# Optimization experiments

Hardware: AMD Instinct MI355X
Metric: run time of the kernel (lower is better)

Reference implementation:

```python
import jax, jax.numpy as jnp
import numpy as np

HID = 256        # constant.hidden_size
EMB = 256        # constant.embedding_size
STATE_NUM = 5    # constant.state_num
PAD_ID = 0


def _lstm(x, Wih, Whh, b):
    # x: (N, T, D) -> (N, T, H); single-layer unidirectional, PyTorch gate order i,f,g,o
    N = x.shape[0]
    Hh = Whh.shape[1]
    def step(carry, xt):
        h, c = carry
        g = xt @ Wih.T + h @ Whh.T + b
        i, f, gg, o = jnp.split(g, 4, axis=-1)
        c = jax.nn.sigmoid(f) * c + jax.nn.sigmoid(i) * jnp.tanh(gg)
        h = jax.nn.sigmoid(o) * jnp.tanh(c)
        return (h, c), h
    h0 = jnp.zeros((N, Hh), x.dtype)
    _, ys = jax.lax.scan(step, (h0, h0), jnp.swapaxes(x, 0, 1))
    return jnp.swapaxes(ys, 0, 1)


def setup_inputs() -> dict:
    rng = np.random.RandomState(0)
    B, L, W, V = 8, 128, 48, 50000
    S = STATE_NUM
    P = L // (S - 1)
    batch_utterances = jnp.asarray(rng.randint(0, V, size=(B, L, W)), jnp.int32)
    utterance_sequence_length = jnp.asarray(rng.randint(1, W + 1, size=(B, L)), jnp.int32)
    perm = np.stack([b * L + rng.permutation(L) for b in range(B)]).reshape(-1)
    session_transpose_matrix = jnp.asarray(perm, jnp.int32)
    stm = np.zeros((B, L, S), np.int32)  # col 0 == 0 -> new-state slot (projection path)
    carry = rng.rand(B, L, S - 1) < 0.3
    pos = rng.randint(1, P + 1, size=(B, L, S - 1))
    stm[:, :, 1:] = np.where(carry, -1, pos)
    state_transition_matrix = jnp.asarray(stm)

    def w(*shape):
        return jnp.asarray(rng.randn(*shape) * 0.05, jnp.float32)

    return dict(
        batch_utterances=batch_utterances,
        utterance_sequence_length=utterance_sequence_length,
        session_transpose_matrix=session_transpose_matrix,
        state_transition_matrix=state_transition_matrix,
        max_conversation_length=L,
        emb=w(V, EMB),
        utt_Wih=w(4 * HID, EMB), utt_Whh=w(4 * HID, HID), utt_b=w(4 * HID),
        ws1=w(HID, HID), ws2=w(1, HID),
        conv_Wih=w(4 * HID, HID), conv_Whh=w(4 * HID, HID), conv_b=w(4 * HID),
        sess_Wih=w(4 * HID, HID), sess_Whh=w(4 * HID, HID), sess_b=w(4 * HID),
        Wp=w(HID, 2 * HID), bp=w(HID),
        Ws=w(HID, 2 * HID), bs=w(HID),
    )


def reference(batch_utterances, utterance_sequence_length, session_transpose_matrix,
              state_transition_matrix, max_conversation_length,
              emb, utt_Wih, utt_Whh, utt_b, ws1, ws2,
              conv_Wih, conv_Whh, conv_b, sess_Wih, sess_Whh, sess_b,
              Wp, bp, Ws, bs):
    B, L, W = batch_utterances.shape
    S = STATE_NUM
    P = L // (S - 1)
    Lc = int(max_conversation_length)

    # --- UtteranceEncoder: embedding lookup + word-level LSTM ---
    tok = batch_utterances.reshape(-1, W)            # (B*L, W)
    word_out = _lstm(emb[tok], utt_Wih, utt_Whh, utt_b)  # (B*L, W, H)

    # --- SelfAttentiveEncoder (1 hop) ---
    hbar = jnp.tanh(word_out @ ws1.T)                # (B*L, W, H)
    logits = (hbar @ ws2.T)[..., 0]                  # (B*L, W)
    logits = logits + (-10000.0) * (tok == PAD_ID).astype(logits.dtype)
    alphas = jax.nn.softmax(logits, axis=1)
    att = jnp.einsum('nw,nwh->nh', alphas, word_out).reshape(B, L, HID)

    # --- ConversationEncoder ---
    conv = _lstm(att, conv_Wih, conv_Whh, conv_b)    # (B, L, H)

    # --- SessionEncoder: gather-permute utterances into sessions, LSTM per session ---
    flat = att.reshape(-1, HID)[session_transpose_matrix]       # (B*L, H)
    sess_in = flat.reshape(B * (S - 1), P, HID)
    sess_out = _lstm(sess_in, sess_Wih, sess_Whh, sess_b).reshape(B, S - 1, P, HID)

    # --- StateMatrixEncoder: sequential scatter/gather scan over conversation steps ---
    sess_idx = jnp.clip(jnp.arange(S) - 1, 0, S - 2)            # (S,)
    gathered = sess_out[:, sess_idx]                            # (B, S, P, H)
    conv_shift = jnp.concatenate([conv[:, :1], conv[:, :L - 1]], axis=1)  # conv_repre[i-1] (i==0 -> [0])
    stm_T = jnp.swapaxes(state_transition_matrix, 0, 1)         # (L, B, S)
    cs_T = jnp.swapaxes(conv_shift, 0, 1)                       # (L, B, H)

    def step(prev_row, inp):
        stm_i, cs = inp                                         # (B,S), (B,H)
        posn = jnp.clip(stm_i - 1, 0, P - 1)
        v_g = jnp.take_along_axis(gathered, posn[:, :, None, None], axis=2)[:, :, 0, :]  # (B,S,H)
        is_carry = (stm_i == -1)[..., None]
        is_gather = (stm_i > 0)[..., None]
        v = jnp.where(is_carry, prev_row, jnp.where(is_gather, v_g, 0.0))
        # AvgPool2d((S-1,1)) over exactly S-1 collected vectors == masked mean
        one_res = jnp.sum(jnp.where(stm_i[..., None] != 0, v, 0.0), axis=1) / (S - 1)
        new0 = jax.nn.relu(jnp.concatenate([one_res, cs], axis=-1) @ Wp.T + bp)
        row = jnp.where(is_gather, v_g, 0.0).at[:, 0, :].set(new0)
        return row, row

    _, rows = jax.lax.scan(step, jnp.zeros((B, S, HID), att.dtype), (stm_T, cs_T))
    state_matrix = jnp.swapaxes(rows, 0, 1)                     # (B, L, S, H)

    # --- ScoresCalculator (unidirectional -> LogSoftmax) ---
    uc = jnp.concatenate([att[:, :Lc], conv[:, :Lc]], axis=-1)  # (B, Lc, 2H)
    up = jax.nn.relu(uc @ Ws.T + bs)                            # (B, Lc, H)
    scores = jnp.einsum('blsh,blh->bls', state_matrix[:, :Lc], up)
    return jax.nn.log_softmax(scores, axis=2)
```

## Files before the change

kernel.cpp:

```cpp
#include <hip/hip_runtime.h>
#include <hip/hip_bf16.h>
#include <math.h>

#define HIDN 256
#define GATES 1024
#define BB 8
#define LLEN 128
#define WLEN 48
#define SNUM 5
#define PLEN 32
#define NSEQ 1024
#define EMBD 256

typedef _Float16 f16;
typedef _Float16 h2_t __attribute__((ext_vector_type(2)));
typedef short short8_t __attribute__((ext_vector_type(8)));
typedef float f32x4 __attribute__((ext_vector_type(4)));

__device__ __forceinline__ float sigf(float x){ return 1.0f/(1.0f+expf(-x)); }

__device__ __forceinline__ unsigned short f2bf(float f){
  unsigned int x = __builtin_bit_cast(unsigned int, f);
  x += 0x7fffu + ((x >> 16) & 1u);
  return (unsigned short)(x >> 16);
}
__device__ __forceinline__ float bf2f(unsigned short u){
  unsigned int x = ((unsigned int)u) << 16;
  return __builtin_bit_cast(float, x);
}

__device__ __forceinline__ float fd2(unsigned int w, unsigned int h, float acc){
  h2_t wa = __builtin_bit_cast(h2_t, w);
  h2_t hb = __builtin_bit_cast(h2_t, h);
#if defined(__has_builtin)
#if __has_builtin(__builtin_amdgcn_fdot2)
  return __builtin_amdgcn_fdot2(wa, hb, acc, false);
#else
  return acc + (float)wa[0]*(float)hb[0] + (float)wa[1]*(float)hb[1];
#endif
#else
  return acc + (float)wa[0]*(float)hb[0] + (float)wa[1]*(float)hb[1];
#endif
}

__device__ __forceinline__ float dot8(uint4 w, uint4 h, float acc){
  acc = fd2(w.x, h.x, acc);
  acc = fd2(w.y, h.y, acc);
  acc = fd2(w.z, h.z, acc);
  acc = fd2(w.w, h.w, acc);
  return acc;
}

template<bool GATHER, bool BIAS, bool RELU, bool SPLIT>
__global__ __launch_bounds__(256) void gemm_abt64_k(
  const float* __restrict__ A, const float* __restrict__ A2,
  const float* __restrict__ Bm, const float* __restrict__ bias,
  float* __restrict__ C, const int* __restrict__ gidx,
  int K, int N, int ostride)
{
  __shared__ float As[32][68];
  __shared__ float Bs[32][68];
  const int tid = threadIdx.x;
  const int m0 = blockIdx.x*64, n0 = blockIdx.y*64;
  const int tx = tid & 15, ty = tid >> 4;
  const int lr = tid >> 3;
  const int lc = (tid & 7) * 4;
  float acc[4][4] = {};
  for (int k0 = 0; k0 < K; k0 += 32){
    #pragma unroll
    for (int hf = 0; hf < 2; ++hf){
      const int r = lr + hf*32;
      int am = m0 + r;
      if (GATHER) am = gidx[am];
      const float* asrc;
      if (SPLIT){
        if (k0 < 256) asrc = A  + (size_t)am*256 + k0 + lc;
        else          asrc = A2 + (size_t)am*256 + (k0-256) + lc;
      } else {
        asrc = A + (size_t)am*K + k0 + lc;
      }
      float4 av = *reinterpret_cast<const float4*>(asrc);
      float4 bv = *reinterpret_cast<const float4*>(Bm + (size_t)(n0+r)*K + k0 + lc);
      As[lc+0][r]=av.x; As[lc+1][r]=av.y; As[lc+2][r]=av.z; As[lc+3][r]=av.w;
      Bs[lc+0][r]=bv.x; Bs[lc+1][r]=bv.y; Bs[lc+2][r]=bv.z; Bs[lc+3][r]=bv.w;
    }
    __syncthreads();
    #pragma unroll
    for (int kk = 0; kk < 32; ++kk){
      const float4 a = *reinterpret_cast<const float4*>(&As[kk][ty*4]);
      const float4 b = *reinterpret_cast<const float4*>(&Bs[kk][tx*4]);
      acc[0][0] += a.x*b.x; acc[0][1] += a.x*b.y; acc[0][2] += a.x*b.z; acc[0][3] += a.x*b.w;
      acc[1][0] += a.y*b.x; acc[1][1] += a.y*b.y; acc[1][2] += a.y*b.z; acc[1][3] += a.y*b.w;
      acc[2][0] += a.z*b.x; acc[2][1] += a.z*b.y; acc[2][2] += a.z*b.z; acc[2][3] += a.z*b.w;
      acc[3][0] += a.w*b.x; acc[3][1] += a.w*b.y; acc[3][2] += a.w*b.z; acc[3][3] += a.w*b.w;
    }
    __syncthreads();
  }
  float4 bb;
  if (BIAS) bb = *reinterpret_cast<const float4*>(bias + n0 + tx*4);
  else      { bb.x=0.f; bb.y=0.f; bb.z=0.f; bb.w=0.f; }
  #pragma unroll
  for (int i = 0; i < 4; ++i){
    float4 o;
    o.x = acc[i][0]+bb.x; o.y = acc[i][1]+bb.y; o.z = acc[i][2]+bb.z; o.w = acc[i][3]+bb.w;
    if (RELU){ o.x=fmaxf(o.x,0.f); o.y=fmaxf(o.y,0.f); o.z=fmaxf(o.z,0.f); o.w=fmaxf(o.w,0.f); }
    *reinterpret_cast<float4*>(C + (size_t)(m0+ty*4+i)*ostride + n0 + tx*4) = o;
  }
}

__global__ __launch_bounds__(256) void cvt_w16_k(
  const float* __restrict__ a, const float* __restrict__ b,
  f16* __restrict__ oa, f16* __restrict__ ob)
{
  const int i = blockIdx.x*256 + threadIdx.x;
  oa[i] = (f16)a[i];
  ob[i] = (f16)b[i];
}

__global__ __launch_bounds__(256) void cvt_bf16_k(
  const float* __restrict__ a, unsigned short* __restrict__ o, int n)
{
  for (int i = blockIdx.x*256 + threadIdx.x; i < n; i += gridDim.x*256)
    o[i] = f2bf(a[i]);
}

__global__ __launch_bounds__(256) void remap_k(const int* __restrict__ tok, int* __restrict__ gidx2){
  const int idx = blockIdx.x*256 + threadIdx.x;
  const int t = idx >> 10, u = idx & 1023;
  gidx2[idx] = tok[u*WLEN + t];
}

__global__ __launch_bounds__(256) void xgemm_k(
  const float* __restrict__ emb, const unsigned short* __restrict__ Wb,
  const float* __restrict__ bias, const int* __restrict__ gidx,
  float* __restrict__ X)
{
  __shared__ char As[32768];
  const int tid = threadIdx.x;
  const int w = tid >> 6, l = tid & 63;
  const int lr = l & 15, lg = l >> 4;
  const int m0 = blockIdx.x*64, n0 = blockIdx.y*64;
  #pragma unroll
  for (int rr = 0; rr < 4; ++rr){
    const int rl = rr*16 + (tid >> 4);
    const int c4 = tid & 15;
    const float* src = emb + (size_t)gidx[m0 + rl]*256;
    const int sw = (rl & 7) << 4;
    #pragma unroll
    for (int q = 0; q < 4; ++q){
      const int idx4 = c4 + q*16;
      float4 v = reinterpret_cast<const float4*>(src)[idx4];
      union { unsigned long long u; unsigned short us[4]; } pk;
      pk.us[0]=f2bf(v.x); pk.us[1]=f2bf(v.y); pk.us[2]=f2bf(v.z); pk.us[3]=f2bf(v.w);
      *reinterpret_cast<unsigned long long*>(As + rl*512 + ((idx4*8) ^ sw)) = pk.u;
    }
  }
  __syncthreads();
  short8_t a[8];
  #pragma unroll
  for (int ks = 0; ks < 8; ++ks){
    const int rl = w*16 + lr;
    a[ks] = *reinterpret_cast<const short8_t*>(As + rl*512 + ((ks*64 + lg*16) ^ ((rl&7)<<4)));
  }
  #pragma unroll
  for (int nt = 0; nt < 4; ++nt){
    f32x4 acc = f32x4{0,0,0,0};
    const int n = n0 + nt*16 + lr;
    #pragma unroll
    for (int ks = 0; ks < 8; ++ks){
      short8_t b = *reinterpret_cast<const short8_t*>(Wb + (size_t)n*256 + ks*32 + lg*8);
      acc = __builtin_amdgcn_mfma_f32_16x16x32_bf16(a[ks], b, acc, 0, 0, 0);
    }
    const float bn = bias[n];
    #pragma unroll
    for (int r = 0; r < 4; ++r){
      const int m = m0 + w*16 + lg*4 + r;
      X[(size_t)m*1024 + n] = acc[r] + bn;
    }
  }
}

__global__ __launch_bounds__(256, 1) void word_stream_k(
  const float* __restrict__ X, const unsigned short* __restrict__ Wb,
  unsigned short* __restrict__ woutb)
{
  extern __shared__ char smem[];
  const int tid = threadIdx.x;
  const int w = tid >> 6, l = tid & 63;
  const int lr = l & 15, lg = l >> 4;
  const int S0 = blockIdx.x * 16;
  char* wlds = smem + w*32768;
  char* hb0 = smem + 131072;
  char* hb1 = smem + 139264;

  #pragma unroll
  for (int rr = 0; rr < 16; ++rr){
    const int rl = rr*4 + lg;
    const unsigned short* src = Wb + (size_t)(768 + w*64 + rl)*256;
    const int sw = (rl & 7) << 4;
    short8_t v0 = *reinterpret_cast<const short8_t*>(src + lr*8);
    short8_t v1 = *reinterpret_cast<const short8_t*>(src + (lr+16)*8);
    *reinterpret_cast<short8_t*>(wlds + rl*512 + ((lr*16) ^ sw)) = v0;
    *reinterpret_cast<short8_t*>(wlds + rl*512 + (((lr+16)*16) ^ sw)) = v1;
  }
  short8_t wr[96];
  #pragma unroll
  for (int g = 0; g < 3; ++g){
    #pragma unroll
    for (int jt = 0; jt < 4; ++jt){
      #pragma unroll
      for (int ks = 0; ks < 8; ++ks){
        const int n = g*256 + w*64 + jt*16 + lr;
        wr[(g*4 + jt)*8 + ks] = *reinterpret_cast<const short8_t*>(
            Wb + (size_t)n*256 + ks*32 + lg*8);
      }
    }
  }
  float c_reg[4][4] = {};
  __syncthreads();

  for (int t = 0; t < WLEN; ++t){
    const char* hr = (t & 1) ? hb1 : hb0;
    char* hw = (t & 1) ? hb0 : hb1;
    #pragma unroll
    for (int jt = 0; jt < 4; ++jt){
      f32x4 acc0 = f32x4{0,0,0,0}, acc1 = f32x4{0,0,0,0};
      f32x4 acc2 = f32x4{0,0,0,0}, acc3 = f32x4{0,0,0,0};
      #pragma unroll
      for (int ks = 0; ks < 8; ++ks){
        short8_t a;
        if (t == 0){
          a = short8_t{0,0,0,0,0,0,0,0};
        } else {
          const int kb = ks*64 + lg*16;
          a = *reinterpret_cast<const short8_t*>(hr + lr*512 + (kb ^ ((lr & 7) << 4)));
        }
        acc0 = __builtin_amdgcn_mfma_f32_16x16x32_bf16(a, wr[(0*4+jt)*8+ks], acc0, 0, 0, 0);
        acc1 = __builtin_amdgcn_mfma_f32_16x16x32_bf16(a, wr[(1*4+jt)*8+ks], acc1, 0, 0, 0);
        acc2 = __builtin_amdgcn_mfma_f32_16x16x32_bf16(a, wr[(2*4+jt)*8+ks], acc2, 0, 0, 0);
        const int rl_o = jt*16 + lr;
        short8_t bo = *reinterpret_cast<const short8_t*>(
            wlds + rl_o*512 + ((ks*64 + lg*16) ^ ((rl_o & 7) << 4)));
        acc3 = __builtin_amdgcn_mfma_f32_16x16x32_bf16(a, bo, acc3, 0, 0, 0);
      }
      const int j = w*64 + jt*16 + lr;
      #pragma unroll
      for (int r = 0; r < 4; ++r){
        const int s = lg*4 + r;
        const float* xp = X + ((size_t)t*1024 + (S0+s))*1024 + j;
        float gi = acc0[r] + xp[0];
        float gf = acc1[r] + xp[256];
        float gg = acc2[r] + xp[512];
        float go = acc3[r] + xp[768];
        float cc = sigf(gf)*c_reg[jt][r] + sigf(gi)*tanhf(gg);
        c_reg[jt][r] = cc;
        float hh = sigf(go)*tanhf(cc);
        unsigned short hb16 = f2bf(hh);
        woutb[((size_t)(S0+s)*WLEN + t)*256 + j] = hb16;
        *reinterpret_cast<unsigned short*>(hw + s*512 + ((j*2) ^ ((s & 7) << 4))) = hb16;
      }
    }
    __syncthreads();
  }
}

__global__ __launch_bounds__(256) void attlog_k(
  const unsigned short* __restrict__ woutb, const unsigned short* __restrict__ ws1b,
  const float* __restrict__ ws2, float* __restrict__ logits)
{
  const int tid = threadIdx.x;
  const int w = tid >> 6, l = tid & 63;
  const int lr = l & 15, lg = l >> 4;
  const int m0 = blockIdx.x*64;
  short8_t a[8];
  #pragma unroll
  for (int ks = 0; ks < 8; ++ks){
    const int m = m0 + w*16 + lr;
    a[ks] = *reinterpret_cast<const short8_t*>(woutb + (size_t)m*256 + ks*32 + lg*8);
  }
  float part[4] = {0.f, 0.f, 0.f, 0.f};
  #pragma unroll
  for (int nt = 0; nt < 16; ++nt){
    f32x4 acc = f32x4{0,0,0,0};
    const int n = nt*16 + lr;
    #pragma unroll
    for (int ks = 0; ks < 8; ++ks){
      short8_t b = *reinterpret_cast<const short8_t*>(ws1b + (size_t)n*256 + ks*32 + lg*8);
      acc = __builtin_amdgcn_mfma_f32_16x16x32_bf16(a[ks], b, acc, 0, 0, 0);
    }
    const float w2 = ws2[n];
    #pragma unroll
    for (int r = 0; r < 4; ++r) part[r] += w2 * tanhf(acc[r]);
  }
  #pragma unroll
  for (int r = 0; r < 4; ++r){
    float p = part[r];
    p += __shfl_xor(p, 1, 64);
    p += __shfl_xor(p, 2, 64);
    p += __shfl_xor(p, 4, 64);
    p += __shfl_xor(p, 8, 64);
    if (lr == 0) logits[m0 + w*16 + lg*4 + r] = p;
  }
}

__global__ __launch_bounds__(256) void att_softmax_k(
  const unsigned short* __restrict__ woutb, const float* __restrict__ logits,
  const int* __restrict__ tok, float* __restrict__ att)
{
  __shared__ float e[WLEN];
  __shared__ float den_s;
  const int n = blockIdx.x, j = threadIdx.x;
  if (j < WLEN){
    float lgt = logits[n*WLEN + j];
    if (tok[n*WLEN + j] == 0) lgt -= 10000.0f;
    e[j] = lgt;
  }
  __syncthreads();
  if (j == 0){
    float mx = -1e30f;
    for (int ww = 0; ww < WLEN; ++ww) mx = fmaxf(mx, e[ww]);
    float den = 0.f;
    for (int ww = 0; ww < WLEN; ++ww){ float ee = expf(e[ww]-mx); e[ww] = ee; den += ee; }
    den_s = den;
  }
  __syncthreads();
  const float inv = 1.0f/den_s;
  float a = 0.f;
  for (int ww = 0; ww < WLEN; ++ww)
    a += e[ww]*bf2f(woutb[((size_t)n*WLEN + ww)*HIDN + j]);
  att[(size_t)n*HIDN + j] = a*inv;
}

__global__ __launch_bounds__(256) void word_gates_k(
    const int* __restrict__ tok, const float* __restrict__ emb,
    const float* __restrict__ Wih, const float* __restrict__ Whh,
    const float* __restrict__ bias, const float* __restrict__ hbuf,
    float* __restrict__ G, int t)
{
  __shared__ float As[32][68];
  __shared__ float Bs[32][68];
  const int tid = threadIdx.x;
  const int m0 = blockIdx.x*64, n0 = blockIdx.y*64;
  const int tx = tid & 15, ty = tid >> 4;
  const int lr = tid >> 3;
  const int lc = (tid & 7) * 4;
  float acc[4][4] = {};
  for (int kt = 0; kt < 16; ++kt){
    const int k0 = (kt & 7)*32;
    const bool xp = (kt < 8);
    #pragma unroll
    for (int hf = 0; hf < 2; ++hf){
      const int r = lr + hf*32;
      float4 av, bv;
      if (xp){
        const int token = tok[(m0+r)*WLEN + t];
        av = *reinterpret_cast<const float4*>(emb + (size_t)token*EMBD + k0 + lc);
      } else {
        av = *reinterpret_cast<const float4*>(hbuf + (size_t)(m0+r)*HIDN + k0 + lc);
      }
      const float* bptr = (xp ? Wih : Whh) + (size_t)(n0+r)*HIDN + k0 + lc;
      bv = *reinterpret_cast<const float4*>(bptr);
      As[lc+0][r]=av.x; As[lc+1][r]=av.y; As[lc+2][r]=av.z; As[lc+3][r]=av.w;
      Bs[lc+0][r]=bv.x; Bs[lc+1][r]=bv.y; Bs[lc+2][r]=bv.z; Bs[lc+3][r]=bv.w;
    }
    __syncthreads();
    #pragma unroll
    for (int kk = 0; kk < 32; ++kk){
      const float4 a = *reinterpret_cast<const float4*>(&As[kk][ty*4]);
      const float4 b = *reinterpret_cast<const float4*>(&Bs[kk][tx*4]);
      acc[0][0] += a.x*b.x; acc[0][1] += a.x*b.y; acc[0][2] += a.x*b.z; acc[0][3] += a.x*b.w;
      acc[1][0] += a.y*b.x; acc[1][1] += a.y*b.y; acc[1][2] += a.y*b.z; acc[1][3] += a.y*b.w;
      acc[2][0] += a.z*b.x; acc[2][1] += a.z*b.y; acc[2][2] += a.z*b.z; acc[2][3] += a.z*b.w;
      acc[3][0] += a.w*b.x; acc[3][1] += a.w*b.y; acc[3][2] += a.w*b.z; acc[3][3] += a.w*b.w;
    }
    __syncthreads();
  }
  const float4 bb = *reinterpret_cast<const float4*>(bias + n0 + tx*4);
  #pragma unroll
  for (int i = 0; i < 4; ++i){
    float4 o;
    o.x = acc[i][0]+bb.x; o.y = acc[i][1]+bb.y; o.z = acc[i][2]+bb.z; o.w = acc[i][3]+bb.w;
    *reinterpret_cast<float4*>(G + (size_t)(m0+ty*4+i)*GATES + n0 + tx*4) = o;
  }
}

__global__ __launch_bounds__(256) void word_update_k(
  const float* __restrict__ G, float* __restrict__ h, float* __restrict__ c,
  unsigned short* __restrict__ woutb, int t)
{
  int idx = blockIdx.x*256 + threadIdx.x;
  int m = idx >> 8, j = idx & 255;
  const float* g = G + (size_t)m*GATES;
  float gi = g[j], gf = g[HIDN+j], gg = g[2*HIDN+j], go = g[3*HIDN+j];
  float cc = c[idx];
  cc = sigf(gf)*cc + sigf(gi)*tanhf(gg);
  float hh = sigf(go)*tanhf(cc);
  c[idx] = cc; h[idx] = hh;
  woutb[(size_t)m*WLEN*HIDN + (size_t)t*HIDN + j] = f2bf(hh);
}

__global__ __launch_bounds__(512, 2) void recur512_k(
  const float* __restrict__ xwc, const f16* __restrict__ w16c, float* __restrict__ convb,
  const float* __restrict__ xws, const f16* __restrict__ w16s, float* __restrict__ soutb)
{
  const float* xw; const f16* w16; float* out; int seq, T;
  if (blockIdx.x < 8){ seq = blockIdx.x;     T = 128; xw = xwc; w16 = w16c; out = convb; }
  else               { seq = blockIdx.x - 8; T = 32;  xw = xws; w16 = w16s; out = soutb; }

  extern __shared__ char smem[];
  uint4* w_lds  = (uint4*)smem;
  float* g_s    = (float*)(smem + 131072);
  f16*   h_half = (f16*)(smem + 131072 + 4096);
  const uint4* h4 = (const uint4*)h_half;

  const int tid = threadIdx.x;
  const int n0 = tid, n1 = tid + 512;

  #pragma unroll
  for (int cth = 0; cth < 8; ++cth){
    w_lds[cth*1024 + n0] = *reinterpret_cast<const uint4*>(w16 + (size_t)n0*HIDN + 192 + cth*8);
    w_lds[cth*1024 + n1] = *reinterpret_cast<const uint4*>(w16 + (size_t)n1*HIDN + 192 + cth*8);
  }
  uint4 wr0[24], wr1[24];
  #pragma unroll
  for (int cth = 0; cth < 24; ++cth){
    wr0[cth] = *reinterpret_cast<const uint4*>(w16 + (size_t)n0*HIDN + cth*8);
    wr1[cth] = *reinterpret_cast<const uint4*>(w16 + (size_t)n1*HIDN + cth*8);
  }
  if (tid < 128) reinterpret_cast<uint4*>(h_half)[tid >> 2] = uint4{0,0,0,0};
  float c_reg = 0.f;
  __syncthreads();

  for (int t = 0; t < T; ++t){
    float acc0 = xw[(size_t)(seq*T + t)*GATES + n0];
    float acc1 = xw[(size_t)(seq*T + t)*GATES + n1];
    float a0=0.f, a1=0.f, a2=0.f, a3=0.f;
    #pragma unroll
    for (int k = 0; k < 24; k += 4){
      const uint4 h0 = h4[k+0], h1 = h4[k+1], h2 = h4[k+2], h3 = h4[k+3];
      a0 = dot8(wr0[k+0], h0, a0);
      a1 = dot8(wr0[k+1], h1, a1);
      a2 = dot8(wr0[k+2], h2, a2);
      a3 = dot8(wr0[k+3], h3, a3);
      acc1 = dot8(wr1[k+0], h0, acc1);
      acc1 = dot8(wr1[k+1], h1, acc1);
      acc1 = dot8(wr1[k+2], h2, acc1);
      acc1 = dot8(wr1[k+3], h3, acc1);
    }
    #pragma unroll
    for (int cth = 0; cth < 8; ++cth){
      const uint4 hv = h4[24 + cth];
      const uint4 w0 = w_lds[cth*1024 + n0];
      const uint4 w1 = w_lds[cth*1024 + n1];
      a0 = dot8(w0, hv, a0);
      acc1 = dot8(w1, hv, acc1);
    }
    g_s[n0] = acc0 + (a0+a1) + (a2+a3);
    g_s[n1] = acc1;
    __syncthreads();
    if (tid < HIDN){
      const int j = tid;
      float gi = g_s[j], gf = g_s[HIDN+j], gg = g_s[2*HIDN+j], go = g_s[3*HIDN+j];
      float cc = sigf(gf)*c_reg + sigf(gi)*tanhf(gg);
      c_reg = cc;
      float hh = sigf(go)*tanhf(cc);
      h_half[j] = (f16)hh;
      out[(size_t)(seq*T + t)*HIDN + j] = hh;
    }
    __syncthreads();
  }
}

__global__ __launch_bounds__(256) void scan_prep_k(
  const float* __restrict__ sess_out, const float* __restrict__ conv_out,
  const int* __restrict__ stm, float* __restrict__ state, float* __restrict__ onec)
{
  const int bl = blockIdx.x;
  const int b = bl >> 7, l = bl & 127;
  const int j = threadIdx.x;
  float ones = 0.f;
  #pragma unroll
  for (int s = 1; s < SNUM; ++s){
    const int sv = stm[(size_t)bl*SNUM + s];
    float vg = 0.f;
    if (sv > 0){
      int p = sv - 1; if (p > PLEN-1) p = PLEN-1;
      vg = sess_out[((size_t)(b*4 + (s-1))*PLEN + p)*HIDN + j];
    }
    float v = vg;
    if (sv == -1){
      v = 0.f;
      if (l > 0){
        const int pv = stm[(size_t)(bl-1)*SNUM + s];
        if (pv > 0){
          int p2 = pv - 1; if (p2 > PLEN-1) p2 = PLEN-1;
          v = sess_out[((size_t)(b*4 + (s-1))*PLEN + p2)*HIDN + j];
        }
      }
    }
    if (sv != 0) ones += v;
    state[((size_t)bl*SNUM + s)*HIDN + j] = vg;
  }
  onec[(size_t)bl*(2*HIDN) + j] = ones * 0.25f;
  const int lp = (l == 0) ? 0 : (l-1);
  onec[(size_t)bl*(2*HIDN) + HIDN + j] = conv_out[((size_t)(b*LLEN + lp))*HIDN + j];
}

__global__ __launch_bounds__(256) void scores_k(
  const float* __restrict__ state, const float* __restrict__ up, float* __restrict__ out)
{
  const int n = blockIdx.x, j = threadIdx.x;
  __shared__ float red[SNUM][4];
  const float u = up[(size_t)n*HIDN + j];
  const int lane = j & 63, wid = j >> 6;
  #pragma unroll
  for (int s = 0; s < SNUM; ++s){
    float p = state[((size_t)n*SNUM + s)*HIDN + j]*u;
    for (int off = 32; off; off >>= 1) p += __shfl_down(p, off, 64);
    if (lane == 0) red[s][wid] = p;
  }
  __syncthreads();
  if (j == 0){
    float sc[SNUM]; float mx = -1e30f;
    #pragma unroll
    for (int s = 0; s < SNUM; ++s){
      sc[s] = red[s][0]+red[s][1]+red[s][2]+red[s][3];
      mx = fmaxf(mx, sc[s]);
    }
    float den = 0.f;
    #pragma unroll
    for (int s = 0; s < SNUM; ++s) den += expf(sc[s]-mx);
    const float ls = logf(den);
    #pragma unroll
    for (int s = 0; s < SNUM; ++s) out[(size_t)n*SNUM + s] = sc[s]-mx-ls;
  }
}

static const size_t OFF_G     = 0;
static const size_t OFF_H     = OFF_G     + 1048576;
static const size_t OFF_C     = OFF_H     + 262144;
static const size_t OFF_ATT   = OFF_C     + 262144;
static const size_t OFF_XWC   = OFF_ATT   + 262144;
static const size_t OFF_XWS   = OFF_XWC   + 1048576;
static const size_t OFF_CONV  = OFF_XWS   + 1048576;
static const size_t OFF_SOUT  = OFF_CONV  + 262144;
static const size_t OFF_STATE = OFF_SOUT  + 262144;
static const size_t OFF_ONEC  = OFF_STATE + 1310720;
static const size_t OFF_UP    = OFF_ONEC  + 524288;
static const size_t OFF_LOG   = OFF_UP    + 262144;
static const size_t OFF_GIDX2 = OFF_LOG   + 49152;
static const size_t OFF_W16C  = OFF_GIDX2 + 49152;
static const size_t OFF_W16S  = OFF_W16C  + 131072;
static const size_t OFF_UWHHB = OFF_W16S  + 131072;
static const size_t OFF_WIHB  = OFF_UWHHB + 131072;
static const size_t OFF_WS1B  = OFF_WIHB  + 131072;
static const size_t OFF_WOUTB = OFF_WS1B  + 32768;
static const size_t OFF_X     = OFF_WOUTB + 6291456;
static const size_t NEED_X_FLOATS = OFF_X + (size_t)49152*1024;

static const size_t WORD_LDS_BYTES  = 131072 + 2*8192;
static const size_t RECUR_LDS_BYTES = 131072 + 4096 + 512;

extern "C" void kernel_launch(void* const* d_in, const int* in_sizes, int n_in,
                              void* d_out, int out_size, void* d_ws, size_t ws_size,
                              hipStream_t stream)
{
  const int*   tok   = (const int*)  d_in[0];
  const int*   perm  = (const int*)  d_in[2];
  const int*   stm   = (const int*)  d_in[3];
  const float* emb   = (const float*)d_in[5];
  const float* uWih  = (const float*)d_in[6];
  const float* uWhh  = (const float*)d_in[7];
  const float* ub    = (const float*)d_in[8];
  const float* ws1   = (const float*)d_in[9];
  const float* ws2   = (const float*)d_in[10];
  const float* cWih  = (const float*)d_in[11];
  const float* cWhh  = (const float*)d_in[12];
  const float* cb    = (const float*)d_in[13];
  const float* sWih  = (const float*)d_in[14];
  const float* sWhh  = (const float*)d_in[15];
  const float* sb    = (const float*)d_in[16];
  const float* Wp    = (const float*)d_in[17];
  const float* bp    = (const float*)d_in[18];
  const float* Ws    = (const float*)d_in[19];
  const float* bs    = (const float*)d_in[20];

  float* wsf    = (float*)d_ws;
  float* G      = wsf + OFF_G;
  float* h      = wsf + OFF_H;
  float* c      = wsf + OFF_C;
  float* att    = wsf + OFF_ATT;
  float* xwc    = wsf + OFF_XWC;
  float* xws    = wsf + OFF_XWS;
  float* convb  = wsf + OFF_CONV;
  float* soutb  = wsf + OFF_SOUT;
  float* statem = wsf + OFF_STATE;
  float* onec   = wsf + OFF_ONEC;
  float* upb    = wsf + OFF_UP;
  float* logits = wsf + OFF_LOG;
  int*   gidx2  = (int*)(wsf + OFF_GIDX2);
  f16*   w16c   = (f16*)(wsf + OFF_W16C);
  f16*   w16s   = (f16*)(wsf + OFF_W16S);
  unsigned short* uwhhb = (unsigned short*)(wsf + OFF_UWHHB);
  unsigned short* wihb  = (unsigned short*)(wsf + OFF_WIHB);
  unsigned short* ws1b  = (unsigned short*)(wsf + OFF_WS1B);
  unsigned short* woutb = (unsigned short*)(wsf + OFF_WOUTB);
  float* X      = wsf + OFF_X;

  const bool useX = ws_size >= NEED_X_FLOATS*sizeof(float);

  hipFuncSetAttribute(reinterpret_cast<const void*>(word_stream_k),
                      hipFuncAttributeMaxDynamicSharedMemorySize, (int)WORD_LDS_BYTES);
  hipFuncSetAttribute(reinterpret_cast<const void*>(recur512_k),
                      hipFuncAttributeMaxDynamicSharedMemorySize, (int)RECUR_LDS_BYTES);

  cvt_w16_k<<<1024, 256, 0, stream>>>(cWhh, sWhh, w16c, w16s);
  cvt_bf16_k<<<256, 256, 0, stream>>>(uWhh, uwhhb, 262144);
  cvt_bf16_k<<<256, 256, 0, stream>>>(uWih, wihb, 262144);
  cvt_bf16_k<<<64, 256, 0, stream>>>(ws1, ws1b, 65536);

  if (useX){
    remap_k<<<192, 256, 0, stream>>>(tok, gidx2);
    xgemm_k<<<dim3(768,16), 256, 0, stream>>>(emb, wihb, ub, gidx2, X);
    word_stream_k<<<64, 256, WORD_LDS_BYTES, stream>>>(X, uwhhb, woutb);
  } else {
    hipMemsetAsync(h, 0, 2*262144*sizeof(float), stream);
    for (int t = 0; t < WLEN; ++t){
      word_gates_k<<<dim3(16,16), 256, 0, stream>>>(tok, emb, uWih, uWhh, ub, h, G, t);
      word_update_k<<<1024, 256, 0, stream>>>(G, h, c, woutb, t);
    }
  }

  attlog_k<<<768, 256, 0, stream>>>(woutb, ws1b, ws2, logits);
  att_softmax_k<<<1024, 256, 0, stream>>>(woutb, logits, tok, att);

  gemm_abt64_k<false,true,false,false><<<dim3(16,16), 256, 0, stream>>>(
    att, nullptr, cWih, cb, xwc, nullptr, 256, GATES, GATES);
  gemm_abt64_k<true,true,false,false><<<dim3(16,16), 256, 0, stream>>>(
    att, nullptr, sWih, sb, xws, perm, 256, GATES, GATES);

  recur512_k<<<40, 512, RECUR_LDS_BYTES, stream>>>(xwc, w16c, convb, xws, w16s, soutb);

  scan_prep_k<<<1024, 256, 0, stream>>>(soutb, convb, stm, statem, onec);
  gemm_abt64_k<false,true,true,false><<<dim3(16,4), 256, 0, stream>>>(
    onec, nullptr, Wp, bp, statem, nullptr, 512, HIDN, SNUM*HIDN);

  gemm_abt64_k<false,true,true,true><<<dim3(16,4), 256, 0, stream>>>(
    att, convb, Ws, bs, upb, nullptr, 512, HIDN, HIDN);
  scores_k<<<1024, 256, 0, stream>>>(statem, upb, (float*)d_out);
}
```

Before: 1.257 ms.

## Batch conversation/session LSTMs onto bf16 MFMA and store word gate inputs in bf16

```diff
diff --git a/kernel.cpp b/kernel.cpp
--- a/kernel.cpp
+++ b/kernel.cpp
@@ -4,16 +4,12 @@
 
 #define HIDN 256
 #define GATES 1024
-#define BB 8
 #define LLEN 128
 #define WLEN 48
 #define SNUM 5
 #define PLEN 32
-#define NSEQ 1024
 #define EMBD 256
 
-typedef _Float16 f16;
-typedef _Float16 h2_t __attribute__((ext_vector_type(2)));
 typedef short short8_t __attribute__((ext_vector_type(8)));
 typedef float f32x4 __attribute__((ext_vector_type(4)));
 
@@ -27,28 +23,6 @@
 __device__ __forceinline__ float bf2f(unsigned short u){
   unsigned int x = ((unsigned int)u) << 16;
   return __builtin_bit_cast(float, x);
-}
-
-__device__ __forceinline__ float fd2(unsigned int w, unsigned int h, float acc){
-  h2_t wa = __builtin_bit_cast(h2_t, w);
-  h2_t hb = __builtin_bit_cast(h2_t, h);
-#if defined(__has_builtin)
-#if __has_builtin(__builtin_amdgcn_fdot2)
-  return __builtin_amdgcn_fdot2(wa, hb, acc, false);
-#else
-  return acc + (float)wa[0]*(float)hb[0] + (float)wa[1]*(float)hb[1];
-#endif
-#else
-  return acc + (float)wa[0]*(float)hb[0] + (float)wa[1]*(float)hb[1];
-#endif
-}
-
-__device__ __forceinline__ float dot8(uint4 w, uint4 h, float acc){
-  acc = fd2(w.x, h.x, acc);
-  acc = fd2(w.y, h.y, acc);
-  acc = fd2(w.z, h.z, acc);
-  acc = fd2(w.w, h.w, acc);
-  return acc;
 }
 
 template<bool GATHER, bool BIAS, bool RELU, bool SPLIT>
@@ -108,16 +82,16 @@
   }
 }
 
-__global__ __launch_bounds__(256) void cvt_w16_k(
+__global__ __launch_bounds__(256) void cvt2_k(
   const float* __restrict__ a, const float* __restrict__ b,
-  f16* __restrict__ oa, f16* __restrict__ ob)
-{
-  const int i = blockIdx.x*256 + threadIdx.x;
-  oa[i] = (f16)a[i];
-  ob[i] = (f16)b[i];
-}
-
-__global__ __launch_bounds__(256) void cvt_bf16_k(
+  unsigned short* __restrict__ oa, unsigned short* __restrict__ ob, int n)
+{
+  for (int i = blockIdx.x*256 + threadIdx.x; i < n; i += gridDim.x*256){
+    oa[i] = f2bf(a[i]);
+    ob[i] = f2bf(b[i]);
+  }
+}
+__global__ __launch_bounds__(256) void cvt1_k(
   const float* __restrict__ a, unsigned short* __restrict__ o, int n)
 {
   for (int i = blockIdx.x*256 + threadIdx.x; i < n; i += gridDim.x*256)
@@ -130,10 +104,11 @@
   gidx2[idx] = tok[u*WLEN + t];
 }
 
-__global__ __launch_bounds__(256) void xgemm_k(
-  const float* __restrict__ emb, const unsigned short* __restrict__ Wb,
+template<int AMODE, bool OUT16>
+__global__ __launch_bounds__(256) void mmabt_k(
+  const void* __restrict__ Asrc, const unsigned short* __restrict__ Wb,
   const float* __restrict__ bias, const int* __restrict__ gidx,
-  float* __restrict__ X)
+  void* __restrict__ Cout)
 {
   __shared__ char As[32768];
   const int tid = threadIdx.x;
@@ -141,18 +116,23 @@
   const int lr = l & 15, lg = l >> 4;
   const int m0 = blockIdx.x*64, n0 = blockIdx.y*64;
   #pragma unroll
-  for (int rr = 0; rr < 4; ++rr){
-    const int rl = rr*16 + (tid >> 4);
-    const int c4 = tid & 15;
-    const float* src = emb + (size_t)gidx[m0 + rl]*256;
-    const int sw = (rl & 7) << 4;
-    #pragma unroll
-    for (int q = 0; q < 4; ++q){
-      const int idx4 = c4 + q*16;
-      float4 v = reinterpret_cast<const float4*>(src)[idx4];
-      union { unsigned long long u; unsigned short us[4]; } pk;
-      pk.us[0]=f2bf(v.x); pk.us[1]=f2bf(v.y); pk.us[2]=f2bf(v.z); pk.us[3]=f2bf(v.w);
-      *reinterpret_cast<unsigned long long*>(As + rl*512 + ((idx4*8) ^ sw)) = pk.u;
+  for (int q = 0; q < 8; ++q){
+    const int ck = tid*8 + q;
+    const int rl = ck >> 5, o16 = ck & 31;
+    int row = m0 + rl;
+    if (AMODE <= 1) row = gidx[row];
+    char* dst = As + rl*512 + ((o16*16) ^ ((rl & 7) << 4));
+    if (AMODE == 0){
+      const float* src = (const float*)Asrc + (size_t)row*256 + o16*8;
+      float4 f0 = *reinterpret_cast<const float4*>(src);
+      float4 f1 = *reinterpret_cast<const float4*>(src + 4);
+      union { short8_t s; unsigned short u[8]; } pk;
+      pk.u[0]=f2bf(f0.x); pk.u[1]=f2bf(f0.y); pk.u[2]=f2bf(f0.z); pk.u[3]=f2bf(f0.w);
+      pk.u[4]=f2bf(f1.x); pk.u[5]=f2bf(f1.y); pk.u[6]=f2bf(f1.z); pk.u[7]=f2bf(f1.w);
+      *reinterpret_cast<short8_t*>(dst) = pk.s;
+    } else {
+      *reinterpret_cast<short8_t*>(dst) = *reinterpret_cast<const short8_t*>(
+          (const unsigned short*)Asrc + (size_t)row*256 + o16*8);
     }
   }
   __syncthreads();
@@ -160,7 +140,7 @@
   #pragma unroll
   for (int ks = 0; ks < 8; ++ks){
     const int rl = w*16 + lr;
-    a[ks] = *reinterpret_cast<const short8_t*>(As + rl*512 + ((ks*64 + lg*16) ^ ((rl&7)<<4)));
+    a[ks] = *reinterpret_cast<const short8_t*>(As + rl*512 + ((ks*64 + lg*16) ^ ((rl & 7) << 4)));
   }
   #pragma unroll
   for (int nt = 0; nt < 4; ++nt){
@@ -175,13 +155,15 @@
     #pragma unroll
     for (int r = 0; r < 4; ++r){
       const int m = m0 + w*16 + lg*4 + r;
-      X[(size_t)m*1024 + n] = acc[r] + bn;
-    }
-  }
-}
-
-__global__ __launch_bounds__(256, 1) void word_stream_k(
-  const float* __restrict__ X, const unsigned short* __restrict__ Wb,
+      if (OUT16) ((unsigned short*)Cout)[(size_t)m*1024 + n] = f2bf(acc[r] + bn);
+      else       ((float*)Cout)[(size_t)m*1024 + n] = acc[r] + bn;
+    }
+  }
+}
+
+__global__ __launch_bounds__(512, 1) void word2_k(
+  const unsigned short* __restrict__ Xb,
+  const unsigned short* __restrict__ Wb,
   unsigned short* __restrict__ woutb)
 {
   extern __shared__ char smem[];
@@ -189,75 +171,189 @@
   const int w = tid >> 6, l = tid & 63;
   const int lr = l & 15, lg = l >> 4;
   const int S0 = blockIdx.x * 16;
-  char* wlds = smem + w*32768;
-  char* hb0 = smem + 131072;
-  char* hb1 = smem + 139264;
-
-  #pragma unroll
-  for (int rr = 0; rr < 16; ++rr){
-    const int rl = rr*4 + lg;
-    const unsigned short* src = Wb + (size_t)(768 + w*64 + rl)*256;
-    const int sw = (rl & 7) << 4;
-    short8_t v0 = *reinterpret_cast<const short8_t*>(src + lr*8);
-    short8_t v1 = *reinterpret_cast<const short8_t*>(src + (lr+16)*8);
-    *reinterpret_cast<short8_t*>(wlds + rl*512 + ((lr*16) ^ sw)) = v0;
-    *reinterpret_cast<short8_t*>(wlds + rl*512 + (((lr+16)*16) ^ sw)) = v1;
-  }
-  short8_t wr[96];
-  #pragma unroll
-  for (int g = 0; g < 3; ++g){
-    #pragma unroll
-    for (int jt = 0; jt < 4; ++jt){
-      #pragma unroll
-      for (int ks = 0; ks < 8; ++ks){
-        const int n = g*256 + w*64 + jt*16 + lr;
-        wr[(g*4 + jt)*8 + ks] = *reinterpret_cast<const short8_t*>(
-            Wb + (size_t)n*256 + ks*32 + lg*8);
-      }
-    }
-  }
-  float c_reg[4][4] = {};
+  char* wlds = smem + w*16384;
+  char* hb0  = smem + 131072;
+  char* hb1  = smem + 139264;
+
+  reinterpret_cast<uint4*>(smem + 131072)[tid] = uint4{0,0,0,0};
+  reinterpret_cast<uint4*>(smem + 131072)[512 + tid] = uint4{0,0,0,0};
+
+  #pragma unroll
+  for (int q = 0; q < 16; ++q){
+    const int ck = l*16 + q;
+    const int rl = ck >> 5, o16 = ck & 31;
+    short8_t v = *reinterpret_cast<const short8_t*>(
+        Wb + (size_t)(768 + w*32 + rl)*256 + o16*8);
+    *reinterpret_cast<short8_t*>(wlds + rl*512 + ((o16*16) ^ ((rl & 7) << 4))) = v;
+  }
+  short8_t wi[2][8], wf[2][8];
+  #pragma unroll
+  for (int jt = 0; jt < 2; ++jt){
+    #pragma unroll
+    for (int ks = 0; ks < 8; ++ks){
+      const int n = w*32 + jt*16 + lr;
+      wi[jt][ks] = *reinterpret_cast<const short8_t*>(Wb + (size_t)n*256 + ks*32 + lg*8);
+      wf[jt][ks] = *reinterpret_cast<const short8_t*>(Wb + (size_t)(256+n)*256 + ks*32 + lg*8);
+    }
+  }
+  const unsigned short* gb0 = Wb + (size_t)(512 + w*32 + lr)*256 + lg*8;
+  const unsigned short* gb1 = Wb + (size_t)(512 + w*32 + 16 + lr)*256 + lg*8;
+  float c_reg[2][4] = {};
   __syncthreads();
 
   for (int t = 0; t < WLEN; ++t){
     const char* hr = (t & 1) ? hb1 : hb0;
     char* hw = (t & 1) ? hb0 : hb1;
-    #pragma unroll
-    for (int jt = 0; jt < 4; ++jt){
-      f32x4 acc0 = f32x4{0,0,0,0}, acc1 = f32x4{0,0,0,0};
-      f32x4 acc2 = f32x4{0,0,0,0}, acc3 = f32x4{0,0,0,0};
+    f32x4 aI[2] = { f32x4{0,0,0,0}, f32x4{0,0,0,0} };
+    f32x4 aF[2] = { f32x4{0,0,0,0}, f32x4{0,0,0,0} };
+    f32x4 aG[2] = { f32x4{0,0,0,0}, f32x4{0,0,0,0} };
+    f32x4 aO[2] = { f32x4{0,0,0,0}, f32x4{0,0,0,0} };
+    short8_t gbf[4][2];
+    #pragma unroll
+    for (int p = 0; p < 4; ++p){
+      gbf[p][0] = *reinterpret_cast<const short8_t*>(gb0 + p*32);
+      gbf[p][1] = *reinterpret_cast<const short8_t*>(gb1 + p*32);
+    }
+    #pragma unroll
+    for (int ks = 0; ks < 8; ++ks){
+      short8_t a = *reinterpret_cast<const short8_t*>(
+          hr + lr*512 + ((ks*64 + lg*16) ^ ((lr & 7) << 4)));
       #pragma unroll
-      for (int ks = 0; ks < 8; ++ks){
-        short8_t a;
-        if (t == 0){
-          a = short8_t{0,0,0,0,0,0,0,0};
-        } else {
-          const int kb = ks*64 + lg*16;
-          a = *reinterpret_cast<const short8_t*>(hr + lr*512 + (kb ^ ((lr & 7) << 4)));
-        }
-        acc0 = __builtin_amdgcn_mfma_f32_16x16x32_bf16(a, wr[(0*4+jt)*8+ks], acc0, 0, 0, 0);
-        acc1 = __builtin_amdgcn_mfma_f32_16x16x32_bf16(a, wr[(1*4+jt)*8+ks], acc1, 0, 0, 0);
-        acc2 = __builtin_amdgcn_mfma_f32_16x16x32_bf16(a, wr[(2*4+jt)*8+ks], acc2, 0, 0, 0);
+      for (int jt = 0; jt < 2; ++jt){
         const int rl_o = jt*16 + lr;
         short8_t bo = *reinterpret_cast<const short8_t*>(
             wlds + rl_o*512 + ((ks*64 + lg*16) ^ ((rl_o & 7) << 4)));
-        acc3 = __builtin_amdgcn_mfma_f32_16x16x32_bf16(a, bo, acc3, 0, 0, 0);
-      }
-      const int j = w*64 + jt*16 + lr;
+        aI[jt] = __builtin_amdgcn_mfma_f32_16x16x32_bf16(a, wi[jt][ks], aI[jt], 0, 0, 0);
+        aF[jt] = __builtin_amdgcn_mfma_f32_16x16x32_bf16(a, wf[jt][ks], aF[jt], 0, 0, 0);
+        aG[jt] = __builtin_amdgcn_mfma_f32_16x16x32_bf16(a, gbf[ks & 3][jt], aG[jt], 0, 0, 0);
+        aO[jt] = __builtin_amdgcn_mfma_f32_16x16x32_bf16(a, bo, aO[jt], 0, 0, 0);
+      }
+      if (ks < 4){
+        gbf[ks & 3][0] = *reinterpret_cast<const short8_t*>(gb0 + (ks+4)*32);
+        gbf[ks & 3][1] = *reinterpret_cast<const short8_t*>(gb1 + (ks+4)*32);
+      }
+    }
+    #pragma unroll
+    for (int jt = 0; jt < 2; ++jt){
+      const int j = w*32 + jt*16 + lr;
       #pragma unroll
       for (int r = 0; r < 4; ++r){
         const int s = lg*4 + r;
-        const float* xp = X + ((size_t)t*1024 + (S0+s))*1024 + j;
-        float gi = acc0[r] + xp[0];
-        float gf = acc1[r] + xp[256];
-        float gg = acc2[r] + xp[512];
-        float go = acc3[r] + xp[768];
+        const unsigned short* xp = Xb + ((size_t)t*1024 + (S0+s))*1024 + j;
+        float gi = aI[jt][r] + bf2f(xp[0]);
+        float gf = aF[jt][r] + bf2f(xp[256]);
+        float gg = aG[jt][r] + bf2f(xp[512]);
+        float go = aO[jt][r] + bf2f(xp[768]);
         float cc = sigf(gf)*c_reg[jt][r] + sigf(gi)*tanhf(gg);
         c_reg[jt][r] = cc;
         float hh = sigf(go)*tanhf(cc);
-        unsigned short hb16 = f2bf(hh);
-        woutb[((size_t)(S0+s)*WLEN + t)*256 + j] = hb16;
-        *reinterpret_cast<unsigned short*>(hw + s*512 + ((j*2) ^ ((s & 7) << 4))) = hb16;
+        unsigned short h16 = f2bf(hh);
+        woutb[((size_t)(S0+s)*WLEN + t)*256 + j] = h16;
+        *reinterpret_cast<unsigned short*>(hw + s*512 + ((j*2) ^ ((s & 7) << 4))) = h16;
+      }
+    }
+    __syncthreads();
+  }
+}
+
+__global__ __launch_bounds__(512, 1) void recur2_k(
+  const float* __restrict__ xwc, const float* __restrict__ xws,
+  const unsigned short* __restrict__ cWb, const unsigned short* __restrict__ sWb,
+  float* __restrict__ convb, float* __restrict__ soutb)
+{
+  extern __shared__ char smem[];
+  int T, nseq; const float* X; const unsigned short* Wb; float* out;
+  if (blockIdx.x == 0){ T = 128; nseq = 8;  X = xwc; Wb = cWb; out = convb; }
+  else {
+    T = 32; nseq = 16;
+    X   = xws   + (size_t)(blockIdx.x-1)*16*32*1024;
+    Wb  = sWb;
+    out = soutb + (size_t)(blockIdx.x-1)*16*32*256;
+  }
+  const int tid = threadIdx.x;
+  const int w = tid >> 6, l = tid & 63;
+  const int lr = l & 15, lg = l >> 4;
+  char* wlds = smem + w*16384;
+  char* hb0  = smem + 131072;
+  char* hb1  = smem + 139264;
+
+  reinterpret_cast<uint4*>(smem + 131072)[tid] = uint4{0,0,0,0};
+  reinterpret_cast<uint4*>(smem + 131072)[512 + tid] = uint4{0,0,0,0};
+
+  #pragma unroll
+  for (int q = 0; q < 16; ++q){
+    const int ck = l*16 + q;
+    const int rl = ck >> 5, o16 = ck & 31;
+    short8_t v = *reinterpret_cast<const short8_t*>(
+        Wb + (size_t)(768 + w*32 + rl)*256 + o16*8);
+    *reinterpret_cast<short8_t*>(wlds + rl*512 + ((o16*16) ^ ((rl & 7) << 4))) = v;
+  }
+  short8_t wi[2][8], wf[2][8];
+  #pragma unroll
+  for (int jt = 0; jt < 2; ++jt){
+    #pragma unroll
+    for (int ks = 0; ks < 8; ++ks){
+      const int n = w*32 + jt*16 + lr;
+      wi[jt][ks] = *reinterpret_cast<const short8_t*>(Wb + (size_t)n*256 + ks*32 + lg*8);
+      wf[jt][ks] = *reinterpret_cast<const short8_t*>(Wb + (size_t)(256+n)*256 + ks*32 + lg*8);
+    }
+  }
+  const unsigned short* gb0 = Wb + (size_t)(512 + w*32 + lr)*256 + lg*8;
+  const unsigned short* gb1 = Wb + (size_t)(512 + w*32 + 16 + lr)*256 + lg*8;
+  float c_reg[2][4] = {};
+  __syncthreads();
+
+  for (int t = 0; t < T; ++t){
+    const char* hr = (t & 1) ? hb1 : hb0;
+    char* hw = (t & 1) ? hb0 : hb1;
+    f32x4 aI[2] = { f32x4{0,0,0,0}, f32x4{0,0,0,0} };
+    f32x4 aF[2] = { f32x4{0,0,0,0}, f32x4{0,0,0,0} };
+    f32x4 aG[2] = { f32x4{0,0,0,0}, f32x4{0,0,0,0} };
+    f32x4 aO[2] = { f32x4{0,0,0,0}, f32x4{0,0,0,0} };
+    short8_t gbf[4][2];
+    #pragma unroll
+    for (int p = 0; p < 4; ++p){
+      gbf[p][0] = *reinterpret_cast<const short8_t*>(gb0 + p*32);
+      gbf[p][1] = *reinterpret_cast<const short8_t*>(gb1 + p*32);
+    }
+    #pragma unroll
+    for (int ks = 0; ks < 8; ++ks){
+      short8_t a = *reinterpret_cast<const short8_t*>(
+          hr + lr*512 + ((ks*64 + lg*16) ^ ((lr & 7) << 4)));
+      #pragma unroll
+      for (int jt = 0; jt < 2; ++jt){
+        const int rl_o = jt*16 + lr;
+        short8_t bo = *reinterpret_cast<const short8_t*>(
+            wlds + rl_o*512 + ((ks*64 + lg*16) ^ ((rl_o & 7) << 4)));
+        aI[jt] = __builtin_amdgcn_mfma_f32_16x16x32_bf16(a, wi[jt][ks], aI[jt], 0, 0, 0);
+        aF[jt] = __builtin_amdgcn_mfma_f32_16x16x32_bf16(a, wf[jt][ks], aF[jt], 0, 0, 0);
+        aG[jt] = __builtin_amdgcn_mfma_f32_16x16x32_bf16(a, gbf[ks & 3][jt], aG[jt], 0, 0, 0);
+        aO[jt] = __builtin_amdgcn_mfma_f32_16x16x32_bf16(a, bo, aO[jt], 0, 0, 0);
+      }
+      if (ks < 4){
+        gbf[ks & 3][0] = *reinterpret_cast<const short8_t*>(gb0 + (ks+4)*32);
+        gbf[ks & 3][1] = *reinterpret_cast<const short8_t*>(gb1 + (ks+4)*32);
+      }
+    }
+    #pragma unroll
+    for (int jt = 0; jt < 2; ++jt){
+      const int j = w*32 + jt*16 + lr;
+      #pragma unroll
+      for (int r = 0; r < 4; ++r){
+        const int s = lg*4 + r;
+        const int scl = (s < nseq) ? s : (nseq - 1);
+        const float* xp = X + (size_t)(scl*T + t)*1024 + j;
+        float gi = aI[jt][r] + xp[0];
+        float gf = aF[jt][r] + xp[256];
+        float gg = aG[jt][r] + xp[512];
+        float go = aO[jt][r] + xp[768];
+        float cc = sigf(gf)*c_reg[jt][r] + sigf(gi)*tanhf(gg);
+        c_reg[jt][r] = cc;
+        float hh = sigf(go)*tanhf(cc);
+        if (s < nseq){
+          out[(size_t)(s*T + t)*256 + j] = hh;
+          *reinterpret_cast<unsigned short*>(hw + s*512 + ((j*2) ^ ((s & 7) << 4))) = f2bf(hh);
+        }
       }
     }
     __syncthreads();
@@ -305,7 +401,7 @@
 
 __global__ __launch_bounds__(256) void att_softmax_k(
   const unsigned short* __restrict__ woutb, const float* __restrict__ logits,
-  const int* __restrict__ tok, float* __restrict__ att)
+  const int* __restrict__ tok, float* __restrict__ att, unsigned short* __restrict__ attb)
 {
   __shared__ float e[WLEN];
   __shared__ float den_s;
@@ -328,7 +424,9 @@
   float a = 0.f;
   for (int ww = 0; ww < WLEN; ++ww)
     a += e[ww]*bf2f(woutb[((size_t)n*WLEN + ww)*HIDN + j]);
-  att[(size_t)n*HIDN + j] = a*inv;
+  a *= inv;
+  att[(size_t)n*HIDN + j] = a;
+  attb[(size_t)n*HIDN + j] = f2bf(a);
 }
 
 __global__ __launch_bounds__(256) void word_gates_k(
@@ -399,78 +497,6 @@
   woutb[(size_t)m*WLEN*HIDN + (size_t)t*HIDN + j] = f2bf(hh);
 }
 
-__global__ __launch_bounds__(512, 2) void recur512_k(
-  const float* __restrict__ xwc, const f16* __restrict__ w16c, float* __restrict__ convb,
-  const float* __restrict__ xws, const f16* __restrict__ w16s, float* __restrict__ soutb)
-{
-  const float* xw; const f16* w16; float* out; int seq, T;
-  if (blockIdx.x < 8){ seq = blockIdx.x;     T = 128; xw = xwc; w16 = w16c; out = convb; }
-  else               { seq = blockIdx.x - 8; T = 32;  xw = xws; w16 = w16s; out = soutb; }
-
-  extern __shared__ char smem[];
-  uint4* w_lds  = (uint4*)smem;
-  float* g_s    = (float*)(smem + 131072);
-  f16*   h_half = (f16*)(smem + 131072 + 4096);
-  const uint4* h4 = (const uint4*)h_half;
-
-  const int tid = threadIdx.x;
-  const int n0 = tid, n1 = tid + 512;
-
-  #pragma unroll
-  for (int cth = 0; cth < 8; ++cth){
-    w_lds[cth*1024 + n0] = *reinterpret_cast<const uint4*>(w16 + (size_t)n0*HIDN + 192 + cth*8);
-    w_lds[cth*1024 + n1] = *reinterpret_cast<const uint4*>(w16 + (size_t)n1*HIDN + 192 + cth*8);
-  }
-  uint4 wr0[24], wr1[24];
-  #pragma unroll
-  for (int cth = 0; cth < 24; ++cth){
-    wr0[cth] = *reinterpret_cast<const uint4*>(w16 + (size_t)n0*HIDN + cth*8);
-    wr1[cth] = *reinterpret_cast<const uint4*>(w16 + (size_t)n1*HIDN + cth*8);
-  }
-  if (tid < 128) reinterpret_cast<uint4*>(h_half)[tid >> 2] = uint4{0,0,0,0};
-  float c_reg = 0.f;
-  __syncthreads();
-
-  for (int t = 0; t < T; ++t){
-    float acc0 = xw[(size_t)(seq*T + t)*GATES + n0];
-    float acc1 = xw[(size_t)(seq*T + t)*GATES + n1];
-    float a0=0.f, a1=0.f, a2=0.f, a3=0.f;
-    #pragma unroll
-    for (int k = 0; k < 24; k += 4){
-      const uint4 h0 = h4[k+0], h1 = h4[k+1], h2 = h4[k+2], h3 = h4[k+3];
-      a0 = dot8(wr0[k+0], h0, a0);
-      a1 = dot8(wr0[k+1], h1, a1);
-      a2 = dot8(wr0[k+2], h2, a2);
-      a3 = dot8(wr0[k+3], h3, a3);
-      acc1 = dot8(wr1[k+0], h0, acc1);
-      acc1 = dot8(wr1[k+1], h1, acc1);
-      acc1 = dot8(wr1[k+2], h2, acc1);
-      acc1 = dot8(wr1[k+3], h3, acc1);
-    }
-    #pragma unroll
-    for (int cth = 0; cth < 8; ++cth){
-      const uint4 hv = h4[24 + cth];
-      const uint4 w0 = w_lds[cth*1024 + n0];
-      const uint4 w1 = w_lds[cth*1024 + n1];
-      a0 = dot8(w0, hv, a0);
-      acc1 = dot8(w1, hv, acc1);
-    }
-    g_s[n0] = acc0 + (a0+a1) + (a2+a3);
-    g_s[n1] = acc1;
-    __syncthreads();
-    if (tid < HIDN){
-      const int j = tid;
-      float gi = g_s[j], gf = g_s[HIDN+j], gg = g_s[2*HIDN+j], go = g_s[3*HIDN+j];
-      float cc = sigf(gf)*c_reg + sigf(gi)*tanhf(gg);
-      c_reg = cc;
-      float hh = sigf(go)*tanhf(cc);
-      h_half[j] = (f16)hh;
-      out[(size_t)(seq*T + t)*HIDN + j] = hh;
-    }
-    __syncthreads();
-  }
-}
-
 __global__ __launch_bounds__(256) void scan_prep_k(
   const float* __restrict__ sess_out, const float* __restrict__ conv_out,
   const int* __restrict__ stm, float* __restrict__ state, float* __restrict__ onec)
@@ -540,7 +566,8 @@
 static const size_t OFF_H     = OFF_G     + 1048576;
 static const size_t OFF_C     = OFF_H     + 262144;
 static const size_t OFF_ATT   = OFF_C     + 262144;
-static const size_t OFF_XWC   = OFF_ATT   + 262144;
+static const size_t OFF_ATTB  = OFF_ATT   + 262144;
+static const size_t OFF_XWC   = OFF_ATTB  + 131072;
 static const size_t OFF_XWS   = OFF_XWC   + 1048576;
 static const size_t OFF_CONV  = OFF_XWS   + 1048576;
 static const size_t OFF_SOUT  = OFF_CONV  + 262144;
@@ -549,17 +576,18 @@
 static const size_t OFF_UP    = OFF_ONEC  + 524288;
 static const size_t OFF_LOG   = OFF_UP    + 262144;
 static const size_t OFF_GIDX2 = OFF_LOG   + 49152;
-static const size_t OFF_W16C  = OFF_GIDX2 + 49152;
-static const size_t OFF_W16S  = OFF_W16C  + 131072;
-static const size_t OFF_UWHHB = OFF_W16S  + 131072;
+static const size_t OFF_UWHHB = OFF_GIDX2 + 49152;
 static const size_t OFF_WIHB  = OFF_UWHHB + 131072;
 static const size_t OFF_WS1B  = OFF_WIHB  + 131072;
-static const size_t OFF_WOUTB = OFF_WS1B  + 32768;
+static const size_t OFF_CWHHB = OFF_WS1B  + 32768;
+static const size_t OFF_SWHHB = OFF_CWHHB + 131072;
+static const size_t OFF_CWIHB = OFF_SWHHB + 131072;
+static const size_t OFF_SWIHB = OFF_CWIHB + 131072;
+static const size_t OFF_WOUTB = OFF_SWIHB + 131072;
 static const size_t OFF_X     = OFF_WOUTB + 6291456;
-static const size_t NEED_X_FLOATS = OFF_X + (size_t)49152*1024;
-
-static const size_t WORD_LDS_BYTES  = 131072 + 2*8192;
-static const size_t RECUR_LDS_BYTES = 131072 + 4096 + 512;
+static const size_t NEED_X_FLOATS = OFF_X + (size_t)49152*512;
+
+static const size_t LSTM_LDS_BYTES = 131072 + 16384;
 
 extern "C" void kernel_launch(void* const* d_in, const int* in_sizes, int n_in,
                               void* d_out, int out_size, void* d_ws, size_t ws_size,
@@ -599,30 +627,33 @@
   float* upb    = wsf + OFF_UP;
   float* logits = wsf + OFF_LOG;
   int*   gidx2  = (int*)(wsf + OFF_GIDX2);
-  f16*   w16c   = (f16*)(wsf + OFF_W16C);
-  f16*   w16s   = (f16*)(wsf + OFF_W16S);
+  unsigned short* attb  = (unsigned short*)(wsf + OFF_ATTB);
   unsigned short* uwhhb = (unsigned short*)(wsf + OFF_UWHHB);
   unsigned short* wihb  = (unsigned short*)(wsf + OFF_WIHB);
   unsigned short* ws1b  = (unsigned short*)(wsf + OFF_WS1B);
+  unsigned short* cwhhb = (unsigned short*)(wsf + OFF_CWHHB);
+  unsigned short* swhhb = (unsigned short*)(wsf + OFF_SWHHB);
+  unsigned short* cwihb = (unsigned short*)(wsf + OFF_CWIHB);
+  unsigned short* swihb = (unsigned short*)(wsf + OFF_SWIHB);
   unsigned short* woutb = (unsigned short*)(wsf + OFF_WOUTB);
-  float* X      = wsf + OFF_X;
+  unsigned short* X16   = (unsigned short*)(wsf + OFF_X);
 
   const bool useX = ws_size >= NEED_X_FLOATS*sizeof(float);
 
-  hipFuncSetAttribute(reinterpret_cast<const void*>(word_stream_k),
-                      hipFuncAttributeMaxDynamicSharedMemorySize, (int)WORD_LDS_BYTES);
-  hipFuncSetAttribute(reinterpret_cast<const void*>(recur512_k),
-                      hipFuncAttributeMaxDynamicSharedMemorySize, (int)RECUR_LDS_BYTES);
-
-  cvt_w16_k<<<1024, 256, 0, stream>>>(cWhh, sWhh, w16c, w16s);
-  cvt_bf16_k<<<256, 256, 0, stream>>>(uWhh, uwhhb, 262144);
-  cvt_bf16_k<<<256, 256, 0, stream>>>(uWih, wihb, 262144);
-  cvt_bf16_k<<<64, 256, 0, stream>>>(ws1, ws1b, 65536);
+  hipFuncSetAttribute(reinterpret_cast<const void*>(word2_k),
+                      hipFuncAttributeMaxDynamicSharedMemorySize, (int)LSTM_LDS_BYTES);
+  hipFuncSetAttribute(reinterpret_cast<const void*>(recur2_k),
+                      hipFuncAttributeMaxDynamicSharedMemorySize, (int)LSTM_LDS_BYTES);
+
+  cvt2_k<<<256, 256, 0, stream>>>(uWhh, uWih, uwhhb, wihb, 262144);
+  cvt2_k<<<256, 256, 0, stream>>>(cWhh, sWhh, cwhhb, swhhb, 262144);
+  cvt2_k<<<256, 256, 0, stream>>>(cWih, sWih, cwihb, swihb, 262144);
+  cvt1_k<<<64, 256, 0, stream>>>(ws1, ws1b, 65536);
 
   if (useX){
     remap_k<<<192, 256, 0, stream>>>(tok, gidx2);
-    xgemm_k<<<dim3(768,16), 256, 0, stream>>>(emb, wihb, ub, gidx2, X);
-    word_stream_k<<<64, 256, WORD_LDS_BYTES, stream>>>(X, uwhhb, woutb);
+    mmabt_k<0,true><<<dim3(768,16), 256, 0, stream>>>(emb, wihb, ub, gidx2, X16);
+    word2_k<<<64, 512, LSTM_LDS_BYTES, stream>>>(X16, uwhhb, woutb);
   } else {
     hipMemsetAsync(h, 0, 2*262144*sizeof(float), stream);
     for (int t = 0; t < WLEN; ++t){
@@ -632,14 +663,12 @@
   }
 
   attlog_k<<<768, 256, 0, stream>>>(woutb, ws1b, ws2, logits);
-  att_softmax_k<<<1024, 256, 0, stream>>>(woutb, logits, tok, att);
-
-  gemm_abt64_k<false,true,false,false><<<dim3(16,16), 256, 0, stream>>>(
-    att, nullptr, cWih, cb, xwc, nullptr, 256, GATES, GATES);
-  gemm_abt64_k<true,true,false,false><<<dim3(16,16), 256, 0, stream>>>(
-    att, nullptr, sWih, sb, xws, perm, 256, GATES, GATES);
-
-  recur512_k<<<40, 512, RECUR_LDS_BYTES, stream>>>(xwc, w16c, convb, xws, w16s, soutb);
+  att_softmax_k<<<1024, 256, 0, stream>>>(woutb, logits, tok, att, attb);
+
+  mmabt_k<2,false><<<dim3(16,16), 256, 0, stream>>>(attb, cwihb, cb, nullptr, xwc);
+  mmabt_k<1,false><<<dim3(16,16), 256, 0, stream>>>(attb, swihb, sb, perm, xws);
+
+  recur2_k<<<3, 512, LSTM_LDS_BYTES, stream>>>(xwc, xws, cwhhb, swhhb, convb, soutb);
 
   scan_prep_k<<<1024, 256, 0, stream>>>(soutb, convb, stm, statem, onec);
   gemm_abt64_k<false,true,true,false><<<dim3(16,4), 256, 0, stream>>>(
```

New measurement: 1.693 ms. 1.35x slower.
